# Kernel optimization log

Hardware: AMD Instinct MI355X
Metric: run time of the kernel (lower is better)

The kernel has to match this reference:

```python
import jax, jax.numpy as jnp
import numpy as np

N = 50000      # nodes per type
E = 600000     # edges per relation
D_IN = 128
D_OUT = 64


def setup_inputs() -> dict:
    key = jax.random.key(0)
    ks = jax.random.split(key, 12)
    x_v0 = jax.random.normal(ks[0], (N, D_IN), dtype=jnp.float32)
    x_v1 = jax.random.normal(ks[1], (N, D_IN), dtype=jnp.float32)
    edge_v0 = jax.random.randint(ks[2], (2, E), 0, N, dtype=jnp.int64)
    edge_v1 = jax.random.randint(ks[3], (2, E), 0, N, dtype=jnp.int64)
    s = 1.0 / np.sqrt(D_IN)
    Wrel0 = jax.random.uniform(ks[4], (D_OUT, D_IN), jnp.float32, -s, s)
    brel0 = jax.random.uniform(ks[5], (D_OUT,), jnp.float32, -s, s)
    Wroot0 = jax.random.uniform(ks[6], (D_OUT, D_IN), jnp.float32, -s, s)
    Wrel1 = jax.random.uniform(ks[7], (D_OUT, D_IN), jnp.float32, -s, s)
    brel1 = jax.random.uniform(ks[8], (D_OUT,), jnp.float32, -s, s)
    Wroot1 = jax.random.uniform(ks[9], (D_OUT, D_IN), jnp.float32, -s, s)
    sf = 1.0 / np.sqrt(2 * D_OUT)
    Wfc = jax.random.uniform(ks[10], (1, 2 * D_OUT), jnp.float32, -sf, sf)
    bfc = jax.random.uniform(ks[11], (1,), jnp.float32, -sf, sf)
    return {"x_v0": x_v0, "x_v1": x_v1, "edge_v0": edge_v0, "edge_v1": edge_v1,
            "Wrel0": Wrel0, "brel0": brel0, "Wroot0": Wroot0,
            "Wrel1": Wrel1, "brel1": brel1, "Wroot1": Wroot1,
            "Wfc": Wfc, "bfc": bfc}


def _graph_conv(x, edge_index, Wrel, brel, Wroot):
    # PyG GraphConv (aggr='add'): out = lin_rel(sum_{j in N(i)} x_j) + lin_root(x_i)
    src, dst = edge_index[0], edge_index[1]
    agg = jax.ops.segment_sum(x[src], dst, num_segments=x.shape[0])  # [N, D_IN]
    return agg @ Wrel.T + brel + x @ Wroot.T


def reference(x_v0, x_v1, edge_v0, edge_v1, Wrel0, brel0, Wroot0,
              Wrel1, brel1, Wroot1, Wfc, bfc):
    h0 = jax.nn.relu(_graph_conv(x_v0, edge_v0, Wrel0, brel0, Wroot0))  # [N, 64]
    h1 = jax.nn.relu(_graph_conv(x_v1, edge_v1, Wrel1, brel1, Wroot1))  # [N, 64]
    h = jnp.concatenate([h0, h1], axis=1)  # [N, 128]
    return h @ Wfc.T + bfc  # [N, 1]
```

## Files before the change

### kernel.cpp

```cpp
#include <hip/hip_runtime.h>
#include <hip/hip_bf16.h>

typedef __attribute__((ext_vector_type(8))) short short8;
typedef __attribute__((ext_vector_type(4))) short short4v;
typedef __attribute__((ext_vector_type(4))) float floatx4;

#define NB    1000
#define BPN   50
#define BCAP  832
#define PBLK  160
#define SCAP  24
#define BM    64

static __device__ __forceinline__ unsigned short bf16_of(float f) {
    union { float f; unsigned u; } v; v.f = f;
    unsigned r = (v.u + 0x7FFF + ((v.u >> 16) & 1)) >> 16;
    return (unsigned short)r;
}
static __device__ __forceinline__ float lo_f(unsigned u) {
    union { float f; unsigned u; } v; v.u = u << 16; return v.f;
}
static __device__ __forceinline__ float hi_f(unsigned u) {
    union { float f; unsigned u; } v; v.u = u & 0xFFFF0000u; return v.f;
}

__global__ __launch_bounds__(256) void convert_w(
    const float* __restrict__ Wrel0, const float* __restrict__ Wroot0,
    const float* __restrict__ Wrel1, const float* __restrict__ Wroot1,
    unsigned short* __restrict__ Wb0, unsigned short* __restrict__ Wb1)
{
    int c = blockIdx.x * 256 + threadIdx.x;
    if (c >= 4096) return;

    const float* s; unsigned short* d;
    if      (c < 1024) { s = Wrel0 + c * 8;           d = Wb0 + c * 8; }
    else if (c < 2048) { int t = c - 1024; s = Wroot0 + t * 8; d = Wb0 + 8192 + t * 8; }
    else if (c < 3072) { int t = c - 2048; s = Wrel1 + t * 8;  d = Wb1 + t * 8; }
    else               { int t = c - 3072; s = Wroot1 + t * 8; d = Wb1 + 8192 + t * 8; }

    floatx4 v0 = *(const floatx4*)s;
    floatx4 v1 = *(const floatx4*)(s + 4);
    short8 r = { (short)bf16_of(v0[0]), (short)bf16_of(v0[1]),
                 (short)bf16_of(v0[2]), (short)bf16_of(v0[3]),
                 (short)bf16_of(v1[0]), (short)bf16_of(v1[1]),
                 (short)bf16_of(v1[2]), (short)bf16_of(v1[3]) };
    *(short8*)d = r;
}

union SmemU {
    struct { short x_sh[BM * 136]; } g;
    struct { int lcur[NB]; } p;
};

__global__ __launch_bounds__(256) void gemm_and_pass(
    const float* __restrict__ X0, const float* __restrict__ X1,
    const unsigned short* __restrict__ Wb0, const unsigned short* __restrict__ Wb1,
    unsigned short* __restrict__ Yrel0, unsigned short* __restrict__ Yrel1,
    unsigned short* __restrict__ Yroot0, unsigned short* __restrict__ Yroot1,
    const int* __restrict__ e0, const int* __restrict__ e1,
    unsigned int* __restrict__ pairs0, unsigned int* __restrict__ pairs1,
    unsigned short* __restrict__ cnt0, unsigned short* __restrict__ cnt1,
    int E, int N)
{
    __shared__ __align__(16) SmemU sm;
    const int tid = threadIdx.x;
    const int rel = blockIdx.y;

    if (blockIdx.x < PBLK) {
        const int* e        = rel ? e1 : e0;
        unsigned int* pairs = rel ? pairs1 : pairs0;
        unsigned short* cnt = rel ? cnt1 : cnt0;
        const int blk       = blockIdx.x;

        const int epb = (E + PBLK - 1) / PBLK;
        const int s0  = blk * epb;
        const int s1  = min(s0 + epb, E);

        for (int b = tid; b < NB; b += 256) sm.p.lcur[b] = 0;
        __syncthreads();

        for (int i = s0 + tid; i < s1; i += 256 * 4) {
            const int i1 = i + 256, i2 = i + 512, i3 = i + 768;
            int d0 = e[E + i];
            int sA = e[i];
            int d1 = (i1 < s1) ? e[E + i1] : -1;
            int sB = (i1 < s1) ? e[i1] : 0;
            int d2 = (i2 < s1) ? e[E + i2] : -1;
            int sC = (i2 < s1) ? e[i2] : 0;
            int d3 = (i3 < s1) ? e[E + i3] : -1;
            int sD = (i3 < s1) ? e[i3] : 0;

#define PROC(dd, ss)                                                         \
            if ((unsigned)(dd) < (unsigned)N) {                              \
                unsigned usrc = ((unsigned)(ss) < (unsigned)N) ? (unsigned)(ss) : 0u; \
                int b_ = (unsigned)(dd) / BPN;                               \
                int pos = atomicAdd(&sm.p.lcur[b_], 1);                      \
                if (pos < SCAP)                                              \
                    pairs[((size_t)blk * NB + b_) * SCAP + pos] =            \
                        ((unsigned)(dd) << 16) | usrc;                       \
            }
            PROC(d0, sA) PROC(d1, sB) PROC(d2, sC) PROC(d3, sD)
#undef PROC
        }
        __syncthreads();

        for (int b = tid; b < NB; b += 256)
            cnt[b * PBLK + blk] = (unsigned short)min(sm.p.lcur[b], SCAP);
        return;
    }

    const float* X           = rel ? X1 : X0;
    const unsigned short* Wb = rel ? Wb1 : Wb0;
    unsigned short* Yrel     = rel ? Yrel1 : Yrel0;
    unsigned short* Yroot    = rel ? Yroot1 : Yroot0;

    const int m0   = (blockIdx.x - PBLK) * BM;
    const int w    = tid >> 6;
    const int lane = tid & 63;
    const int q    = lane >> 4;
    const int r    = lane & 15;

    short8 bw[2][4];
#pragma unroll
    for (int nt = 0; nt < 2; ++nt)
#pragma unroll
        for (int ko = 0; ko < 4; ++ko)
            bw[nt][ko] = *(const short8*)(Wb + (w * 32 + nt * 16 + r) * 128 + ko * 32 + q * 8);

#pragma unroll
    for (int i = 0; i < 8; ++i) {
        int c    = tid + 256 * i;
        int row  = c >> 5;
        int f    = (c & 31) * 4;
        int node = m0 + row;
        floatx4 v = {};
        if (node < N) v = *(const floatx4*)(X + (size_t)node * 128 + f);
        short4v sv = { (short)bf16_of(v[0]), (short)bf16_of(v[1]),
                       (short)bf16_of(v[2]), (short)bf16_of(v[3]) };
        *(short4v*)&sm.g.x_sh[row * 136 + f] = sv;
    }
    __syncthreads();

    floatx4 acc[4][2] = {};
#pragma unroll
    for (int ko = 0; ko < 4; ++ko) {
        int kb = ko * 32 + q * 8;
        short8 a[4];
#pragma unroll
        for (int mt = 0; mt < 4; ++mt)
            a[mt] = *(const short8*)&sm.g.x_sh[(mt * 16 + r) * 136 + kb];
#pragma unroll
        for (int mt = 0; mt < 4; ++mt) {
            acc[mt][0] = __builtin_amdgcn_mfma_f32_16x16x32_bf16(a[mt], bw[0][ko], acc[mt][0], 0, 0, 0);
            acc[mt][1] = __builtin_amdgcn_mfma_f32_16x16x32_bf16(a[mt], bw[1][ko], acc[mt][1], 0, 0, 0);
        }
    }

    unsigned short* Yp = (w < 2) ? Yrel : Yroot;
    const int cbase = (w & 1) * 32;
#pragma unroll
    for (int mt = 0; mt < 4; ++mt)
#pragma unroll
        for (int nt = 0; nt < 2; ++nt) {
            int col = cbase + nt * 16 + r;
#pragma unroll
            for (int reg = 0; reg < 4; ++reg) {
                int node = m0 + mt * 16 + q * 4 + reg;
                if (node < N) Yp[(size_t)node * 64 + col] = bf16_of(acc[mt][nt][reg]);
            }
        }
}

__global__ __launch_bounds__(512) void bucket_gather(
    const unsigned int* __restrict__ pairs0, const unsigned int* __restrict__ pairs1,
    const unsigned short* __restrict__ cnt0, const unsigned short* __restrict__ cnt1,
    const unsigned short* __restrict__ Yrel0, const unsigned short* __restrict__ Yrel1,
    const unsigned short* __restrict__ Yroot0, const unsigned short* __restrict__ Yroot1,
    const float* __restrict__ brel0, const float* __restrict__ brel1,
    const float* __restrict__ wfc, const float* __restrict__ bfc,
    float* __restrict__ out, int N)
{
    __shared__ unsigned short slist0[BCAP], slist1[BCAP];
    __shared__ int pref0[PBLK + 1], pref1[PBLK + 1];
    __shared__ int cnt0s[BPN], cnt1s[BPN];
    __shared__ int off0s[BPN], off1s[BPN];
    __shared__ int cur0s[BPN], cur1s[BPN];

    const int tid  = threadIdx.x;
    const int b    = blockIdx.x;
    const int wv   = tid >> 6;
    const int lane = tid & 63;
    const int c    = lane & 31;
    const int half = lane >> 5;

    for (int i = tid; i < BPN; i += 512) { cnt0s[i] = 0; cnt1s[i] = 0; }

    if (wv == 0) {
        int cv[3], ssum = 0;
#pragma unroll
        for (int t = 0; t < 3; ++t) {
            int idx = lane * 3 + t;
            cv[t] = (idx < PBLK) ? (int)cnt0[b * PBLK + idx] : 0;
            ssum += cv[t];
        }
        int inc = ssum;
#pragma unroll
        for (int d = 1; d < 64; d <<= 1) {
            int t = __shfl_up(inc, d, 64);
            if (lane >= d) inc += t;
        }
        int ex = inc - ssum;
#pragma unroll
        for (int t = 0; t < 3; ++t) {
            int idx = lane * 3 + t;
            if (idx <= PBLK) pref0[idx] = ex;
            ex += cv[t];
        }
    } else if (wv == 1) {
        int cv[3], ssum = 0;
#pragma unroll
        for (int t = 0; t < 3; ++t) {
            int idx = lane * 3 + t;
            cv[t] = (idx < PBLK) ? (int)cnt1[b * PBLK + idx] : 0;
            ssum += cv[t];
        }
        int inc = ssum;
#pragma unroll
        for (int d = 1; d < 64; d <<= 1) {
            int t = __shfl_up(inc, d, 64);
            if (lane >= d) inc += t;
        }
        int ex = inc - ssum;
#pragma unroll
        for (int t = 0; t < 3; ++t) {
            int idx = lane * 3 + t;
            if (idx <= PBLK) pref1[idx] = ex;
            ex += cv[t];
        }
    }
    __syncthreads();

    const unsigned base = (unsigned)(b * BPN);
    const int tot0 = pref0[PBLK];
    const int tot1 = pref1[PBLK];

    for (int j = tid; j < tot0; j += 512) {
        int lo = 0, hi = PBLK;
#pragma unroll
        for (int it = 0; it < 8; ++it) {
            int mid = (lo + hi) >> 1;
            if (pref0[mid] <= j) lo = mid; else hi = mid;
        }
        unsigned p = pairs0[((size_t)lo * NB + b) * SCAP + (j - pref0[lo])];
        atomicAdd(&cnt0s[(p >> 16) - base], 1);
    }
    for (int j = tid; j < tot1; j += 512) {
        int lo = 0, hi = PBLK;
#pragma unroll
        for (int it = 0; it < 8; ++it) {
            int mid = (lo + hi) >> 1;
            if (pref1[mid] <= j) lo = mid; else hi = mid;
        }
        unsigned p = pairs1[((size_t)lo * NB + b) * SCAP + (j - pref1[lo])];
        atomicAdd(&cnt1s[(p >> 16) - base], 1);
    }
    __syncthreads();

    if (wv == 0) {
        int cc = (lane < BPN) ? cnt0s[lane] : 0;
        int inc = cc;
#pragma unroll
        for (int d = 1; d < 64; d <<= 1) {
            int t = __shfl_up(inc, d, 64);
            if (lane >= d) inc += t;
        }
        if (lane < BPN) { off0s[lane] = inc - cc; cur0s[lane] = inc - cc; }
    } else if (wv == 1) {
        int cc = (lane < BPN) ? cnt1s[lane] : 0;
        int inc = cc;
#pragma unroll
        for (int d = 1; d < 64; d <<= 1) {
            int t = __shfl_up(inc, d, 64);
            if (lane >= d) inc += t;
        }
        if (lane < BPN) { off1s[lane] = inc - cc; cur1s[lane] = inc - cc; }
    }
    __syncthreads();

    for (int j = tid; j < tot0; j += 512) {
        int lo = 0, hi = PBLK;
#pragma unroll
        for (int it = 0; it < 8; ++it) {
            int mid = (lo + hi) >> 1;
            if (pref0[mid] <= j) lo = mid; else hi = mid;
        }
        unsigned p = pairs0[((size_t)lo * NB + b) * SCAP + (j - pref0[lo])];
        int pos = atomicAdd(&cur0s[(p >> 16) - base], 1);
        if (pos < BCAP) slist0[pos] = (unsigned short)(p & 0xFFFFu);
    }
    for (int j = tid; j < tot1; j += 512) {
        int lo = 0, hi = PBLK;
#pragma unroll
        for (int it = 0; it < 8; ++it) {
            int mid = (lo + hi) >> 1;
            if (pref1[mid] <= j) lo = mid; else hi = mid;
        }
        unsigned p = pairs1[((size_t)lo * NB + b) * SCAP + (j - pref1[lo])];
        int pos = atomicAdd(&cur1s[(p >> 16) - base], 1);
        if (pos < BCAP) slist1[pos] = (unsigned short)(p & 0xFFFFu);
    }
    __syncthreads();

    const float2 br0 = ((const float2*)brel0)[c];
    const float2 br1 = ((const float2*)brel1)[c];
    const float2 w0  = ((const float2*)wfc)[c];
    const float2 w1  = ((const float2*)(wfc + 64))[c];
    const float bias = bfc[0];

    for (int nl = wv; nl < BPN; nl += 8) {
        int i = b * BPN + nl;
        float a0x = 0.f, a0y = 0.f, a1x = 0.f, a1y = 0.f;

        {
            int st = off0s[nl], d = cnt0s[nl], j = 0;
            for (; j + 7 < d; j += 8) {
                int i0 = slist0[st + j + half];
                int i1 = slist0[st + j + 2 + half];
                int i2 = slist0[st + j + 4 + half];
                int i3 = slist0[st + j + 6 + half];
                unsigned u0 = ((const unsigned*)(Yrel0 + ((size_t)i0 << 6)))[c];
                unsigned u1 = ((const unsigned*)(Yrel0 + ((size_t)i1 << 6)))[c];
                unsigned u2 = ((const unsigned*)(Yrel0 + ((size_t)i2 << 6)))[c];
                unsigned u3 = ((const unsigned*)(Yrel0 + ((size_t)i3 << 6)))[c];
                a0x += (lo_f(u0) + lo_f(u1)) + (lo_f(u2) + lo_f(u3));
                a0y += (hi_f(u0) + hi_f(u1)) + (hi_f(u2) + hi_f(u3));
            }
            for (; j < d; j += 2) {
                int jj = j + half;
                int idx = slist0[st + (jj < d ? jj : d - 1)];
                unsigned u = ((const unsigned*)(Yrel0 + ((size_t)idx << 6)))[c];
                if (jj < d) { a0x += lo_f(u); a0y += hi_f(u); }
            }
        }
        {
            int st = off1s[nl], d = cnt1s[nl], j = 0;
            for (; j + 7 < d; j += 8) {
                int i0 = slist1[st + j + half];
                int i1 = slist1[st + j + 2 + half];
                int i2 = slist1[st + j + 4 + half];
                int i3 = slist1[st + j + 6 + half];
                unsigned u0 = ((const unsigned*)(Yrel1 + ((size_t)i0 << 6)))[c];
                unsigned u1 = ((const unsigned*)(Yrel1 + ((size_t)i1 << 6)))[c];
                unsigned u2 = ((const unsigned*)(Yrel1 + ((size_t)i2 << 6)))[c];
                unsigned u3 = ((const unsigned*)(Yrel1 + ((size_t)i3 << 6)))[c];
                a1x += (lo_f(u0) + lo_f(u1)) + (lo_f(u2) + lo_f(u3));
                a1y += (hi_f(u0) + hi_f(u1)) + (hi_f(u2) + hi_f(u3));
            }
            for (; j < d; j += 2) {
                int jj = j + half;
                int idx = slist1[st + (jj < d ? jj : d - 1)];
                unsigned u = ((const unsigned*)(Yrel1 + ((size_t)idx << 6)))[c];
                if (jj < d) { a1x += lo_f(u); a1y += hi_f(u); }
            }
        }

        a0x += __shfl_xor(a0x, 32, 64);
        a0y += __shfl_xor(a0y, 32, 64);
        a1x += __shfl_xor(a1x, 32, 64);
        a1y += __shfl_xor(a1y, 32, 64);

        unsigned ur0 = ((const unsigned*)(Yroot0 + ((size_t)i << 6)))[c];
        unsigned ur1 = ((const unsigned*)(Yroot1 + ((size_t)i << 6)))[c];

        float h0x = fmaxf(a0x + br0.x + lo_f(ur0), 0.f);
        float h0y = fmaxf(a0y + br0.y + hi_f(ur0), 0.f);
        float h1x = fmaxf(a1x + br1.x + lo_f(ur1), 0.f);
        float h1y = fmaxf(a1y + br1.y + hi_f(ur1), 0.f);
        float s = h0x * w0.x + h0y * w0.y + h1x * w1.x + h1y * w1.y;

#pragma unroll
        for (int m = 16; m > 0; m >>= 1) s += __shfl_xor(s, m, 64);
        if (lane == 0) out[i] = s + bias;
    }
}

extern "C" void kernel_launch(void* const* d_in, const int* in_sizes, int n_in,
                              void* d_out, int out_size, void* d_ws, size_t ws_size,
                              hipStream_t stream)
{
    const int N = in_sizes[0] / 128;
    const int E = in_sizes[2] / 2;

    const float* x0     = (const float*)d_in[0];
    const float* x1     = (const float*)d_in[1];
    const int*   e0     = (const int*)d_in[2];
    const int*   e1     = (const int*)d_in[3];
    const float* Wrel0  = (const float*)d_in[4];
    const float* brel0  = (const float*)d_in[5];
    const float* Wroot0 = (const float*)d_in[6];
    const float* Wrel1  = (const float*)d_in[7];
    const float* brel1  = (const float*)d_in[8];
    const float* Wroot1 = (const float*)d_in[9];
    const float* wfc    = (const float*)d_in[10];
    const float* bfc    = (const float*)d_in[11];
    float* out = (float*)d_out;

    unsigned short* Wb0    = (unsigned short*)d_ws;
    unsigned short* Wb1    = Wb0 + 128 * 128;
    unsigned short* Yrel0  = Wb1 + 128 * 128;
    unsigned short* Yrel1  = Yrel0 + (size_t)N * 64;
    unsigned short* Yroot0 = Yrel1 + (size_t)N * 64;
    unsigned short* Yroot1 = Yroot0 + (size_t)N * 64;
    unsigned int* pairs0   = (unsigned int*)(Yroot1 + (size_t)N * 64);
    unsigned int* pairs1   = pairs0 + (size_t)PBLK * NB * SCAP;
    unsigned short* cnt0   = (unsigned short*)(pairs1 + (size_t)PBLK * NB * SCAP);
    unsigned short* cnt1   = cnt0 + (size_t)NB * PBLK;

    convert_w<<<16, 256, 0, stream>>>(Wrel0, Wroot0, Wrel1, Wroot1, Wb0, Wb1);

    const int gemm_nblk = (N + BM - 1) / BM;
    dim3 fused_grid(PBLK + gemm_nblk, 2);
    gemm_and_pass<<<fused_grid, 256, 0, stream>>>(
        x0, x1, Wb0, Wb1, Yrel0, Yrel1, Yroot0, Yroot1,
        e0, e1, pairs0, pairs1, cnt0, cnt1, E, N);

    bucket_gather<<<NB, 512, 0, stream>>>(pairs0, pairs1, cnt0, cnt1,
                                          Yrel0, Yrel1, Yroot0, Yroot1,
                                          brel0, brel1, wfc, bfc, out, N);
}
```

Measured before the change: 182.2 us.

## Fuse weight bf16 conversion into GEMM, drop LDS staging, shrink edge partitions

Removes the separate weight-conversion kernel. Each GEMM wave now loads fp32 weights and converts them to bf16 in registers. The X tile is loaded and converted straight into MFMA operand registers instead of being staged through shared memory, which drops the LDS round trip and a barrier but duplicates some global loads across waves. The edge-binning pass now uses 64 partitions with a per-bucket capacity of 32 (was 160 and 24), and the count array is transposed. This lets the gather kernel build its prefix sums with a single-element-per-lane scan and a shorter binary search, at the cost of less parallelism in the binning phase.

New measurement: 189.8 us. 4.1% more time.

```diff
diff --git a/kernel.cpp b/kernel.cpp
--- a/kernel.cpp
+++ b/kernel.cpp
@@ -2,14 +2,13 @@
 #include <hip/hip_bf16.h>
 
 typedef __attribute__((ext_vector_type(8))) short short8;
-typedef __attribute__((ext_vector_type(4))) short short4v;
 typedef __attribute__((ext_vector_type(4))) float floatx4;
 
 #define NB    1000
 #define BPN   50
 #define BCAP  832
-#define PBLK  160
-#define SCAP  24
+#define PBLK  64
+#define SCAP  32
 #define BM    64
 
 static __device__ __forceinline__ unsigned short bf16_of(float f) {
@@ -23,38 +22,18 @@
 static __device__ __forceinline__ float hi_f(unsigned u) {
     union { float f; unsigned u; } v; v.u = u & 0xFFFF0000u; return v.f;
 }
-
-__global__ __launch_bounds__(256) void convert_w(
-    const float* __restrict__ Wrel0, const float* __restrict__ Wroot0,
-    const float* __restrict__ Wrel1, const float* __restrict__ Wroot1,
-    unsigned short* __restrict__ Wb0, unsigned short* __restrict__ Wb1)
-{
-    int c = blockIdx.x * 256 + threadIdx.x;
-    if (c >= 4096) return;
-
-    const float* s; unsigned short* d;
-    if      (c < 1024) { s = Wrel0 + c * 8;           d = Wb0 + c * 8; }
-    else if (c < 2048) { int t = c - 1024; s = Wroot0 + t * 8; d = Wb0 + 8192 + t * 8; }
-    else if (c < 3072) { int t = c - 2048; s = Wrel1 + t * 8;  d = Wb1 + t * 8; }
-    else               { int t = c - 3072; s = Wroot1 + t * 8; d = Wb1 + 8192 + t * 8; }
-
-    floatx4 v0 = *(const floatx4*)s;
-    floatx4 v1 = *(const floatx4*)(s + 4);
+static __device__ __forceinline__ short8 cvt8(floatx4 v0, floatx4 v1) {
     short8 r = { (short)bf16_of(v0[0]), (short)bf16_of(v0[1]),
                  (short)bf16_of(v0[2]), (short)bf16_of(v0[3]),
                  (short)bf16_of(v1[0]), (short)bf16_of(v1[1]),
                  (short)bf16_of(v1[2]), (short)bf16_of(v1[3]) };
-    *(short8*)d = r;
-}
-
-union SmemU {
-    struct { short x_sh[BM * 136]; } g;
-    struct { int lcur[NB]; } p;
-};
+    return r;
+}
 
 __global__ __launch_bounds__(256) void gemm_and_pass(
     const float* __restrict__ X0, const float* __restrict__ X1,
-    const unsigned short* __restrict__ Wb0, const unsigned short* __restrict__ Wb1,
+    const float* __restrict__ Wrel0, const float* __restrict__ Wroot0,
+    const float* __restrict__ Wrel1, const float* __restrict__ Wroot1,
     unsigned short* __restrict__ Yrel0, unsigned short* __restrict__ Yrel1,
     unsigned short* __restrict__ Yroot0, unsigned short* __restrict__ Yroot1,
     const int* __restrict__ e0, const int* __restrict__ e1,
@@ -62,7 +41,7 @@
     unsigned short* __restrict__ cnt0, unsigned short* __restrict__ cnt1,
     int E, int N)
 {
-    __shared__ __align__(16) SmemU sm;
+    __shared__ int lcur[NB];
     const int tid = threadIdx.x;
     const int rel = blockIdx.y;
 
@@ -76,7 +55,7 @@
         const int s0  = blk * epb;
         const int s1  = min(s0 + epb, E);
 
-        for (int b = tid; b < NB; b += 256) sm.p.lcur[b] = 0;
+        for (int b = tid; b < NB; b += 256) lcur[b] = 0;
         __syncthreads();
 
         for (int i = s0 + tid; i < s1; i += 256 * 4) {
@@ -94,7 +73,7 @@
             if ((unsigned)(dd) < (unsigned)N) {                              \
                 unsigned usrc = ((unsigned)(ss) < (unsigned)N) ? (unsigned)(ss) : 0u; \
                 int b_ = (unsigned)(dd) / BPN;                               \
-                int pos = atomicAdd(&sm.p.lcur[b_], 1);                      \
+                int pos = atomicAdd(&lcur[b_], 1);                           \
                 if (pos < SCAP)                                              \
                     pairs[((size_t)blk * NB + b_) * SCAP + pos] =            \
                         ((unsigned)(dd) << 16) | usrc;                       \
@@ -105,14 +84,15 @@
         __syncthreads();
 
         for (int b = tid; b < NB; b += 256)
-            cnt[b * PBLK + blk] = (unsigned short)min(sm.p.lcur[b], SCAP);
+            cnt[blk * NB + b] = (unsigned short)min(lcur[b], SCAP);
         return;
     }
 
-    const float* X           = rel ? X1 : X0;
-    const unsigned short* Wb = rel ? Wb1 : Wb0;
-    unsigned short* Yrel     = rel ? Yrel1 : Yrel0;
-    unsigned short* Yroot    = rel ? Yroot1 : Yroot0;
+    const float* X       = rel ? X1 : X0;
+    const float* WrelF   = rel ? Wrel1 : Wrel0;
+    const float* WrootF  = rel ? Wroot1 : Wroot0;
+    unsigned short* Yrel  = rel ? Yrel1 : Yrel0;
+    unsigned short* Yroot = rel ? Yroot1 : Yroot0;
 
     const int m0   = (blockIdx.x - PBLK) * BM;
     const int w    = tid >> 6;
@@ -120,41 +100,44 @@
     const int q    = lane >> 4;
     const int r    = lane & 15;
 
+    const float* Wsrc = (w < 2) ? WrelF : WrootF;
     short8 bw[2][4];
 #pragma unroll
-    for (int nt = 0; nt < 2; ++nt)
-#pragma unroll
-        for (int ko = 0; ko < 4; ++ko)
-            bw[nt][ko] = *(const short8*)(Wb + (w * 32 + nt * 16 + r) * 128 + ko * 32 + q * 8);
-
-#pragma unroll
-    for (int i = 0; i < 8; ++i) {
-        int c    = tid + 256 * i;
-        int row  = c >> 5;
-        int f    = (c & 31) * 4;
-        int node = m0 + row;
-        floatx4 v = {};
-        if (node < N) v = *(const floatx4*)(X + (size_t)node * 128 + f);
-        short4v sv = { (short)bf16_of(v[0]), (short)bf16_of(v[1]),
-                       (short)bf16_of(v[2]), (short)bf16_of(v[3]) };
-        *(short4v*)&sm.g.x_sh[row * 136 + f] = sv;
-    }
-    __syncthreads();
+    for (int nt = 0; nt < 2; ++nt) {
+        const float* wp = Wsrc + ((w & 1) * 32 + nt * 16 + r) * 128;
+#pragma unroll
+        for (int ko = 0; ko < 4; ++ko) {
+            floatx4 v0 = *(const floatx4*)(wp + ko * 32 + q * 8);
+            floatx4 v1 = *(const floatx4*)(wp + ko * 32 + q * 8 + 4);
+            bw[nt][ko] = cvt8(v0, v1);
+        }
+    }
+
+    short8 a[4][4];
+#pragma unroll
+    for (int mt = 0; mt < 4; ++mt) {
+        int node = m0 + mt * 16 + r;
+        const float* xp = X + (size_t)node * 128;
+        bool ok = node < N;
+#pragma unroll
+        for (int ko = 0; ko < 4; ++ko) {
+            floatx4 v0 = {}, v1 = {};
+            if (ok) {
+                v0 = *(const floatx4*)(xp + ko * 32 + q * 8);
+                v1 = *(const floatx4*)(xp + ko * 32 + q * 8 + 4);
+            }
+            a[mt][ko] = cvt8(v0, v1);
+        }
+    }
 
     floatx4 acc[4][2] = {};
 #pragma unroll
-    for (int ko = 0; ko < 4; ++ko) {
-        int kb = ko * 32 + q * 8;
-        short8 a[4];
-#pragma unroll
-        for (int mt = 0; mt < 4; ++mt)
-            a[mt] = *(const short8*)&sm.g.x_sh[(mt * 16 + r) * 136 + kb];
+    for (int ko = 0; ko < 4; ++ko)
 #pragma unroll
         for (int mt = 0; mt < 4; ++mt) {
-            acc[mt][0] = __builtin_amdgcn_mfma_f32_16x16x32_bf16(a[mt], bw[0][ko], acc[mt][0], 0, 0, 0);
-            acc[mt][1] = __builtin_amdgcn_mfma_f32_16x16x32_bf16(a[mt], bw[1][ko], acc[mt][1], 0, 0, 0);
-        }
-    }
+            acc[mt][0] = __builtin_amdgcn_mfma_f32_16x16x32_bf16(a[mt][ko], bw[0][ko], acc[mt][0], 0, 0, 0);
+            acc[mt][1] = __builtin_amdgcn_mfma_f32_16x16x32_bf16(a[mt][ko], bw[1][ko], acc[mt][1], 0, 0, 0);
+        }
 
     unsigned short* Yp = (w < 2) ? Yrel : Yroot;
     const int cbase = (w & 1) * 32;
@@ -196,47 +179,25 @@
     for (int i = tid; i < BPN; i += 512) { cnt0s[i] = 0; cnt1s[i] = 0; }
 
     if (wv == 0) {
-        int cv[3], ssum = 0;
-#pragma unroll
-        for (int t = 0; t < 3; ++t) {
-            int idx = lane * 3 + t;
-            cv[t] = (idx < PBLK) ? (int)cnt0[b * PBLK + idx] : 0;
-            ssum += cv[t];
-        }
-        int inc = ssum;
+        int cc = (int)cnt0[lane * NB + b];
+        int inc = cc;
 #pragma unroll
         for (int d = 1; d < 64; d <<= 1) {
             int t = __shfl_up(inc, d, 64);
             if (lane >= d) inc += t;
         }
-        int ex = inc - ssum;
-#pragma unroll
-        for (int t = 0; t < 3; ++t) {
-            int idx = lane * 3 + t;
-            if (idx <= PBLK) pref0[idx] = ex;
-            ex += cv[t];
-        }
+        if (lane == 0) pref0[0] = 0;
+        pref0[lane + 1] = inc;
     } else if (wv == 1) {
-        int cv[3], ssum = 0;
-#pragma unroll
-        for (int t = 0; t < 3; ++t) {
-            int idx = lane * 3 + t;
-            cv[t] = (idx < PBLK) ? (int)cnt1[b * PBLK + idx] : 0;
-            ssum += cv[t];
-        }
-        int inc = ssum;
+        int cc = (int)cnt1[lane * NB + b];
+        int inc = cc;
 #pragma unroll
         for (int d = 1; d < 64; d <<= 1) {
             int t = __shfl_up(inc, d, 64);
             if (lane >= d) inc += t;
         }
-        int ex = inc - ssum;
-#pragma unroll
-        for (int t = 0; t < 3; ++t) {
-            int idx = lane * 3 + t;
-            if (idx <= PBLK) pref1[idx] = ex;
-            ex += cv[t];
-        }
+        if (lane == 0) pref1[0] = 0;
+        pref1[lane + 1] = inc;
     }
     __syncthreads();
 
@@ -247,7 +208,7 @@
     for (int j = tid; j < tot0; j += 512) {
         int lo = 0, hi = PBLK;
 #pragma unroll
-        for (int it = 0; it < 8; ++it) {
+        for (int it = 0; it < 6; ++it) {
             int mid = (lo + hi) >> 1;
             if (pref0[mid] <= j) lo = mid; else hi = mid;
         }
@@ -257,7 +218,7 @@
     for (int j = tid; j < tot1; j += 512) {
         int lo = 0, hi = PBLK;
 #pragma unroll
-        for (int it = 0; it < 8; ++it) {
+        for (int it = 0; it < 6; ++it) {
             int mid = (lo + hi) >> 1;
             if (pref1[mid] <= j) lo = mid; else hi = mid;
         }
@@ -290,7 +251,7 @@
     for (int j = tid; j < tot0; j += 512) {
         int lo = 0, hi = PBLK;
 #pragma unroll
-        for (int it = 0; it < 8; ++it) {
+        for (int it = 0; it < 6; ++it) {
             int mid = (lo + hi) >> 1;
             if (pref0[mid] <= j) lo = mid; else hi = mid;
         }
@@ -301,7 +262,7 @@
     for (int j = tid; j < tot1; j += 512) {
         int lo = 0, hi = PBLK;
 #pragma unroll
-        for (int it = 0; it < 8; ++it) {
+        for (int it = 0; it < 6; ++it) {
             int mid = (lo + hi) >> 1;
             if (pref1[mid] <= j) lo = mid; else hi = mid;
         }
@@ -405,9 +366,7 @@
     const float* bfc    = (const float*)d_in[11];
     float* out = (float*)d_out;
 
-    unsigned short* Wb0    = (unsigned short*)d_ws;
-    unsigned short* Wb1    = Wb0 + 128 * 128;
-    unsigned short* Yrel0  = Wb1 + 128 * 128;
+    unsigned short* Yrel0  = (unsigned short*)d_ws;
     unsigned short* Yrel1  = Yrel0 + (size_t)N * 64;
     unsigned short* Yroot0 = Yrel1 + (size_t)N * 64;
     unsigned short* Yroot1 = Yroot0 + (size_t)N * 64;
@@ -416,12 +375,11 @@
     unsigned short* cnt0   = (unsigned short*)(pairs1 + (size_t)PBLK * NB * SCAP);
     unsigned short* cnt1   = cnt0 + (size_t)NB * PBLK;
 
-    convert_w<<<16, 256, 0, stream>>>(Wrel0, Wroot0, Wrel1, Wroot1, Wb0, Wb1);
-
     const int gemm_nblk = (N + BM - 1) / BM;
     dim3 fused_grid(PBLK + gemm_nblk, 2);
     gemm_and_pass<<<fused_grid, 256, 0, stream>>>(
-        x0, x1, Wb0, Wb1, Yrel0, Yrel1, Yroot0, Yroot1,
+        x0, x1, Wrel0, Wroot0, Wrel1, Wroot1,
+        Yrel0, Yrel1, Yroot0, Yroot1,
         e0, e1, pairs0, pairs1, cnt0, cnt1, E, N);
 
     bucket_gather<<<NB, 512, 0, stream>>>(pairs0, pairs1, cnt0, cnt1,
```

## Stage bucket edge pairs in LDS once and shrink partition block count

Applied to the files above, without the earlier changes.

The partition phase now uses 64 partition blocks with 32-entry slots instead of 160 with 24, and stores counts in partition-major order so the gather kernel can read one count per lane. The gather kernel copies each bucket's pairs into shared-memory edge lists in a single pass that also counts per node. The second pass reads from LDS, which removes the per-edge binary searches and the repeated global reads of pairs. Fewer partition blocks means more edges per block and per slot, which raises the overflow risk at the SCAP cap and adds LDS use that may lower occupancy. A clamp on the slist range is added to guard overflow.

Result: faster. 173.2 us (-5.0%).

```diff
diff --git a/kernel.cpp b/kernel.cpp
--- a/kernel.cpp
+++ b/kernel.cpp
@@ -7,9 +7,9 @@
 
 #define NB    1000
 #define BPN   50
-#define BCAP  832
-#define PBLK  160
-#define SCAP  24
+#define BCAP  1024
+#define PBLK  64
+#define SCAP  32
 #define BM    64
 
 static __device__ __forceinline__ unsigned short bf16_of(float f) {
@@ -105,7 +105,7 @@
         __syncthreads();
 
         for (int b = tid; b < NB; b += 256)
-            cnt[b * PBLK + blk] = (unsigned short)min(sm.p.lcur[b], SCAP);
+            cnt[blk * NB + b] = (unsigned short)min(sm.p.lcur[b], SCAP);
         return;
     }
 
@@ -180,6 +180,8 @@
     const float* __restrict__ wfc, const float* __restrict__ bfc,
     float* __restrict__ out, int N)
 {
+    __shared__ unsigned elist0[PBLK * SCAP];
+    __shared__ unsigned elist1[PBLK * SCAP];
     __shared__ unsigned short slist0[BCAP], slist1[BCAP];
     __shared__ int pref0[PBLK + 1], pref1[PBLK + 1];
     __shared__ int cnt0s[BPN], cnt1s[BPN];
@@ -196,47 +198,25 @@
     for (int i = tid; i < BPN; i += 512) { cnt0s[i] = 0; cnt1s[i] = 0; }
 
     if (wv == 0) {
-        int cv[3], ssum = 0;
-#pragma unroll
-        for (int t = 0; t < 3; ++t) {
-            int idx = lane * 3 + t;
-            cv[t] = (idx < PBLK) ? (int)cnt0[b * PBLK + idx] : 0;
-            ssum += cv[t];
-        }
-        int inc = ssum;
+        int cc = (int)cnt0[lane * NB + b];
+        int inc = cc;
 #pragma unroll
         for (int d = 1; d < 64; d <<= 1) {
             int t = __shfl_up(inc, d, 64);
             if (lane >= d) inc += t;
         }
-        int ex = inc - ssum;
-#pragma unroll
-        for (int t = 0; t < 3; ++t) {
-            int idx = lane * 3 + t;
-            if (idx <= PBLK) pref0[idx] = ex;
-            ex += cv[t];
-        }
+        if (lane == 0) pref0[0] = 0;
+        pref0[lane + 1] = inc;
     } else if (wv == 1) {
-        int cv[3], ssum = 0;
-#pragma unroll
-        for (int t = 0; t < 3; ++t) {
-            int idx = lane * 3 + t;
-            cv[t] = (idx < PBLK) ? (int)cnt1[b * PBLK + idx] : 0;
-            ssum += cv[t];
-        }
-        int inc = ssum;
+        int cc = (int)cnt1[lane * NB + b];
+        int inc = cc;
 #pragma unroll
         for (int d = 1; d < 64; d <<= 1) {
             int t = __shfl_up(inc, d, 64);
             if (lane >= d) inc += t;
         }
-        int ex = inc - ssum;
-#pragma unroll
-        for (int t = 0; t < 3; ++t) {
-            int idx = lane * 3 + t;
-            if (idx <= PBLK) pref1[idx] = ex;
-            ex += cv[t];
-        }
+        if (lane == 0) pref1[0] = 0;
+        pref1[lane + 1] = inc;
     }
     __syncthreads();
 
@@ -244,25 +224,19 @@
     const int tot0 = pref0[PBLK];
     const int tot1 = pref1[PBLK];
 
-    for (int j = tid; j < tot0; j += 512) {
-        int lo = 0, hi = PBLK;
-#pragma unroll
-        for (int it = 0; it < 8; ++it) {
-            int mid = (lo + hi) >> 1;
-            if (pref0[mid] <= j) lo = mid; else hi = mid;
-        }
-        unsigned p = pairs0[((size_t)lo * NB + b) * SCAP + (j - pref0[lo])];
-        atomicAdd(&cnt0s[(p >> 16) - base], 1);
-    }
-    for (int j = tid; j < tot1; j += 512) {
-        int lo = 0, hi = PBLK;
-#pragma unroll
-        for (int it = 0; it < 8; ++it) {
-            int mid = (lo + hi) >> 1;
-            if (pref1[mid] <= j) lo = mid; else hi = mid;
-        }
-        unsigned p = pairs1[((size_t)lo * NB + b) * SCAP + (j - pref1[lo])];
-        atomicAdd(&cnt1s[(p >> 16) - base], 1);
+    for (int j = tid; j < 2 * PBLK * SCAP; j += 512) {
+        int r1f = j >= PBLK * SCAP;
+        int jj  = r1f ? j - PBLK * SCAP : j;
+        int s   = jj >> 5, k = jj & 31;
+        const int* pr = r1f ? pref1 : pref0;
+        int st = pr[s];
+        int cs = pr[s + 1] - st;
+        if (k < cs) {
+            unsigned p = (r1f ? pairs1 : pairs0)[(((size_t)s * NB + b) << 5) + k];
+            (r1f ? elist1 : elist0)[st + k] = p;
+            int* cp = r1f ? cnt1s : cnt0s;
+            atomicAdd(&cp[(p >> 16) - base], 1);
+        }
     }
     __syncthreads();
 
@@ -288,24 +262,12 @@
     __syncthreads();
 
     for (int j = tid; j < tot0; j += 512) {
-        int lo = 0, hi = PBLK;
-#pragma unroll
-        for (int it = 0; it < 8; ++it) {
-            int mid = (lo + hi) >> 1;
-            if (pref0[mid] <= j) lo = mid; else hi = mid;
-        }
-        unsigned p = pairs0[((size_t)lo * NB + b) * SCAP + (j - pref0[lo])];
+        unsigned p = elist0[j];
         int pos = atomicAdd(&cur0s[(p >> 16) - base], 1);
         if (pos < BCAP) slist0[pos] = (unsigned short)(p & 0xFFFFu);
     }
     for (int j = tid; j < tot1; j += 512) {
-        int lo = 0, hi = PBLK;
-#pragma unroll
-        for (int it = 0; it < 8; ++it) {
-            int mid = (lo + hi) >> 1;
-            if (pref1[mid] <= j) lo = mid; else hi = mid;
-        }
-        unsigned p = pairs1[((size_t)lo * NB + b) * SCAP + (j - pref1[lo])];
+        unsigned p = elist1[j];
         int pos = atomicAdd(&cur1s[(p >> 16) - base], 1);
         if (pos < BCAP) slist1[pos] = (unsigned short)(p & 0xFFFFu);
     }
@@ -322,7 +284,9 @@
         float a0x = 0.f, a0y = 0.f, a1x = 0.f, a1y = 0.f;
 
         {
-            int st = off0s[nl], d = cnt0s[nl], j = 0;
+            int st = off0s[nl], d = cnt0s[nl];
+            if (st + d > BCAP) d = (st < BCAP) ? (BCAP - st) : 0;
+            int j = 0;
             for (; j + 7 < d; j += 8) {
                 int i0 = slist0[st + j + half];
                 int i1 = slist0[st + j + 2 + half];
@@ -343,7 +307,9 @@
             }
         }
         {
-            int st = off1s[nl], d = cnt1s[nl], j = 0;
+            int st = off1s[nl], d = cnt1s[nl];
+            if (st + d > BCAP) d = (st < BCAP) ? (BCAP - st) : 0;
+            int j = 0;
             for (; j + 7 < d; j += 8) {
                 int i0 = slist1[st + j + half];
                 int i1 = slist1[st + j + 2 + half];
```
